# Kernel tuning notes

Measured on AMD Instinct MI355X. Metric: run time of the kernel, lower is better.

The kernel has to match this reference:

```python
import jax, jax.numpy as jnp
import numpy as np

N = 16384          # nodes
E = 262144         # edges (before self-loops)
FIN_N, FIN_E = 768, 64
F, FE = 256, 128   # node/edge channels
H, C = 8, 32       # heads, per-head dim (H*C == F)
L = 2              # num GATv2 modules
NEG_SLOPE = 0.2


def layer_norm(x, g, b, eps=1e-5):
    mu = jnp.mean(x, axis=-1, keepdims=True)
    var = jnp.mean((x - mu) ** 2, axis=-1, keepdims=True)
    return (x - mu) * jax.lax.rsqrt(var + eps) * g + b


def segment_softmax(logits, seg, n):
    # logits: [Et, H], seg: [Et] destination node ids
    m = jax.ops.segment_max(logits, seg, num_segments=n)
    m = jnp.where(jnp.isfinite(m), m, 0.0)
    e = jnp.exp(logits - m[seg])
    s = jax.ops.segment_sum(e, seg, num_segments=n)
    return e / (s[seg] + 1e-16)


def setup_inputs() -> dict:
    key = jax.random.key(0)
    ks = jax.random.split(key, 20)
    inp = {
        "node_feats": jax.random.normal(ks[0], (N, FIN_N), jnp.float32),
        "edge_index": jax.random.randint(ks[1], (2, E), 0, N, dtype=jnp.int32),
        "edge_attr": jax.random.normal(ks[2], (E, FIN_E), jnp.float32),
        # input projections (bias=False)
        "init_node_w": jax.random.normal(ks[3], (F, FIN_N), jnp.float32) * 0.02,
        "init_edge_w": jax.random.normal(ks[4], (FE, FIN_E), jnp.float32) * 0.02,
        # per-layer GATv2 params, stacked on leading layer dim L
        "lin_l_w": jax.random.normal(ks[5], (L, H * C, F), jnp.float32) * 0.05,
        "lin_l_b": jnp.zeros((L, H * C), jnp.float32),
        "lin_r_w": jax.random.normal(ks[6], (L, H * C, F), jnp.float32) * 0.05,
        "lin_r_b": jnp.zeros((L, H * C), jnp.float32),
        "lin_edge_w": jax.random.normal(ks[7], (L, H * C, FE), jnp.float32) * 0.05,
        "att": jax.random.normal(ks[8], (L, H, C), jnp.float32) * 0.05,
        "gat_bias": jnp.zeros((L, H * C), jnp.float32),
        # block params
        "ln1_g": jnp.ones((L, F), jnp.float32), "ln1_b": jnp.zeros((L, F), jnp.float32),
        "mlp_w1": jax.random.normal(ks[9], (L, 2 * F, F), jnp.float32) * 0.05,
        "mlp_w2": jax.random.normal(ks[10], (L, F, 2 * F), jnp.float32) * 0.05,
        "ln2_g": jnp.ones((L, F), jnp.float32), "ln2_b": jnp.zeros((L, F), jnp.float32),
    }
    return inp


def _gatv2_module(x, src, dst, e_emb, p, l, n):
    # e_emb: [Et, H, C] already projected edge embeddings (incl. self-loops)
    x_l = (x @ p["lin_l_w"][l].T + p["lin_l_b"][l]).reshape(n, H, C)
    x_r = (x @ p["lin_r_w"][l].T + p["lin_r_b"][l]).reshape(n, H, C)
    m = x_l[src] + x_r[dst] + e_emb                    # [Et, H, C]
    g = jnp.where(m >= 0, m, NEG_SLOPE * m)            # leaky_relu(0.2)
    logits = jnp.einsum('ehc,hc->eh', g, p["att"][l])
    alpha = segment_softmax(logits, dst, n)            # [Et, H]
    out = jax.ops.segment_sum(alpha[:, :, None] * x_l[src], dst, num_segments=n)
    out = out.reshape(n, H * C) + p["gat_bias"][l]
    # residual -> LN -> MLP -> residual -> LN  (dropout=0, eval mode)
    h = layer_norm(x + out, p["ln1_g"][l], p["ln1_b"][l])
    y = jax.nn.gelu(h @ p["mlp_w1"][l].T, approximate=False) @ p["mlp_w2"][l].T
    return layer_norm(h + y, p["ln2_g"][l], p["ln2_b"][l])


def reference(node_feats, edge_index, edge_attr, init_node_w, init_edge_w,
              lin_l_w, lin_l_b, lin_r_w, lin_r_b, lin_edge_w, att, gat_bias,
              ln1_g, ln1_b, mlp_w1, mlp_w2, ln2_g, ln2_b):
    p = dict(lin_l_w=lin_l_w, lin_l_b=lin_l_b, lin_r_w=lin_r_w, lin_r_b=lin_r_b,
             lin_edge_w=lin_edge_w, att=att, gat_bias=gat_bias, ln1_g=ln1_g,
             ln1_b=ln1_b, mlp_w1=mlp_w1, mlp_w2=mlp_w2, ln2_g=ln2_g, ln2_b=ln2_b)
    x = node_feats @ init_node_w.T                     # [N, F]
    ea = edge_attr @ init_edge_w.T                     # [E, FE]
    src, dst = edge_index[0], edge_index[1]
    # add self loops with fill_value='mean' (mean of incoming edge_attr per node)
    cnt = jax.ops.segment_sum(jnp.ones((E,), ea.dtype), dst, num_segments=N)
    loop_attr = jax.ops.segment_sum(ea, dst, num_segments=N) / jnp.maximum(cnt, 1.0)[:, None]
    ea_all = jnp.concatenate([ea, loop_attr], axis=0)  # [E+N, FE]
    ar = jnp.arange(N, dtype=src.dtype)
    src_all = jnp.concatenate([src, ar])
    dst_all = jnp.concatenate([dst, ar])
    for l in range(L):
        e_emb = (ea_all @ lin_edge_w[l].T).reshape(-1, H, C)
        x = _gatv2_module(x, src_all, dst_all, e_emb, p, l, N)
    return x
```

## Files before the change

### kernel.cpp

```cpp
#include <hip/hip_runtime.h>

typedef unsigned short u16;
typedef __attribute__((ext_vector_type(8))) short s8v;
typedef __attribute__((ext_vector_type(4))) float f4v;

#define NN 16384
#define EE 262144
#define ET (EE + NN)
#define NTILES (ET / 64)

__device__ __forceinline__ float bfu(u16 h){ return __uint_as_float((unsigned)h << 16); }
__device__ __forceinline__ u16 f2bf(float f){
  unsigned u = __float_as_uint(f);
  unsigned r = u + 0x7FFFu + ((u >> 16) & 1u);
  return (u16)(r >> 16);
}
__device__ __forceinline__ float ldf(const void* p, size_t i, int isbf){
  return isbf ? bfu(((const u16*)p)[i]) : ((const float*)p)[i];
}
__device__ __forceinline__ float gelu_f(float x){ return 0.5f*x*(1.0f+erff(x*0.7071067811865475f)); }

__device__ __forceinline__ uint4 load8bf(const void* p, size_t eoff, int isbf){
  if (isbf) return *(const uint4*)((const u16*)p + eoff);
  const float* f = (const float*)p + eoff;
  uint4 r;
  r.x = (unsigned)f2bf(f[0]) | ((unsigned)f2bf(f[1])<<16);
  r.y = (unsigned)f2bf(f[2]) | ((unsigned)f2bf(f[3])<<16);
  r.z = (unsigned)f2bf(f[4]) | ((unsigned)f2bf(f[5])<<16);
  r.w = (unsigned)f2bf(f[6]) | ((unsigned)f2bf(f[7])<<16);
  return r;
}

__device__ __forceinline__ void gload16(const void* g, void* l){
  __builtin_amdgcn_global_load_lds((const __attribute__((address_space(1))) void*)g,
                                   (__attribute__((address_space(3))) void*)l, 16, 0, 0);
}

__global__ void k_detect(const void* nf, int* flag)
{
  int t = threadIdx.x;
  const float* f = (const float*)nf;
  int cnt = 0;
  for (int i = t; i < 4096; i += 256) {
    float a = fabsf(f[i]);
    if (a > 1e-5f && a < 100.0f) cnt++;
  }
  __shared__ int s[256];
  s[t] = cnt; __syncthreads();
  for (int st = 128; st > 0; st >>= 1) { if (t < st) s[t] += s[t+st]; __syncthreads(); }
  if (t == 0) *flag = (s[0] < 2048) ? 1 : 0;
}

__global__ void k_cvt(const void* __restrict__ in, u16* __restrict__ out, const int* __restrict__ dflag)
{
  int isbf = *dflag;
  size_t i = ((size_t)blockIdx.x*256 + threadIdx.x)*8;
  *(uint4*)&out[i] = load8bf(in, i, isbf);
}

__global__ void k_wcvt(const void* __restrict__ lw, const void* __restrict__ rw,
                       const void* __restrict__ w1, const void* __restrict__ w2,
                       const void* __restrict__ iw, u16* __restrict__ wall,
                       const int* __restrict__ dflag)
{
  int isbf = *dflag;
  size_t i = ((size_t)blockIdx.x*256 + threadIdx.x)*8;
  const void* src; size_t off;
  if (i < 196608) { src = iw; off = i; }
  else {
    size_t j = i - 196608;
    size_t l = j / 393216; j -= l*393216;
    if (j < 65536)       { src = lw; off = l*65536 + j; }
    else if (j < 131072) { src = rw; off = l*65536 + (j - 65536); }
    else if (j < 262144) { src = w1; off = l*131072 + (j - 131072); }
    else                 { src = w2; off = l*131072 + (j - 262144); }
  }
  *(uint4*)&wall[i] = load8bf(src, off, isbf);
}

template<int KK, int NJ, int ACT, int CFMT>
__global__ __launch_bounds__(256)
void mg4(const u16* __restrict__ A, const u16* __restrict__ B,
         const void* __restrict__ bias1, const void* __restrict__ bias2,
         size_t bioff, int nsplit, int has_bias,
         void* __restrict__ C, void* __restrict__ C2, int N,
         const int* __restrict__ dflag)
{
  __shared__ u16 As[32][512];
  int isbf = *dflag;
  int t = threadIdx.x;
  int w = t>>6, lane = t&63, l4 = lane&15, quad = lane>>4;

  int nwg = gridDim.x*gridDim.y;
  int wg  = blockIdx.y*gridDim.x + blockIdx.x;
  int lg  = (wg & 7)*(nwg >> 3) + (wg >> 3);
  int bx  = lg % gridDim.x, by = lg / gridDim.x;
  int bm = by*64, bn = bx*(64*NJ);

  const u16* gA = A + (size_t)(bm + w*16 + l4)*KK + quad*8;
  const u16* gB[NJ];
  #pragma unroll
  for (int j=0;j<NJ;++j)
    gB[j] = B + (size_t)(bn + (NJ*w + j)*16 + l4)*KK + quad*8;

  f4v acc[4][NJ];
  f4v zero = {0.f,0.f,0.f,0.f};
  #pragma unroll
  for (int i=0;i<4;++i)
    #pragma unroll
    for (int j=0;j<NJ;++j) acc[i][j] = zero;

  #pragma unroll
  for (int kc=0; kc<KK/256; ++kc) {
    if (kc) __syncthreads();
    s8v breg[8][NJ];
    #pragma unroll
    for (int c=0;c<8;++c)
      #pragma unroll
      for (int j=0;j<NJ;++j)
        breg[c][j] = *(const s8v*)(gB[j] + kc*256 + c*32);
    #pragma unroll
    for (int c=0;c<8;++c)
      gload16(gA + kc*256 + c*32, &As[c*4 + w][0]);
    __syncthreads();
    #pragma unroll
    for (int c=0;c<8;++c) {
      s8v a[4];
      #pragma unroll
      for (int i=0;i<4;++i) a[i] = *(const s8v*)&As[c*4 + i][lane*8];
      #pragma unroll
      for (int i=0;i<4;++i)
        #pragma unroll
        for (int j=0;j<NJ;++j)
          acc[i][j] = __builtin_amdgcn_mfma_f32_16x16x32_bf16(a[i], breg[c][j], acc[i][j], 0,0,0);
    }
  }

  #pragma unroll
  for (int i=0;i<4;++i)
    #pragma unroll
    for (int j=0;j<NJ;++j) {
      int cj = bn + (NJ*w + j)*16 + l4;
      float bvs = 0.f;
      if (has_bias) bvs = (cj < nsplit) ? ldf(bias1, bioff + cj, isbf)
                                        : ldf(bias2, bioff + cj - nsplit, isbf);
      #pragma unroll
      for (int r=0;r<4;++r) {
        int row = bm + i*16 + quad*4 + r;
        float v = acc[i][j][r] + bvs;
        if (ACT==1) v = gelu_f(v);
        if (CFMT==1) ((u16*)C)[(size_t)row*N + cj] = f2bf(v);
        else {
          ((float*)C)[(size_t)row*N + cj] = v;
          if (CFMT==2) ((u16*)C2)[(size_t)row*N + cj] = f2bf(v);
        }
      }
    }
}

__global__ void k_count(const int* __restrict__ dst, int* __restrict__ deg)
{
  int e = blockIdx.x*256 + threadIdx.x;
  if (e >= ET) return;
  int d = (e < EE) ? dst[e] : (e - EE);
  atomicAdd(&deg[d], 1);
}

__global__ void k_scan(const int* __restrict__ deg, int* __restrict__ rowstart)
{
  __shared__ int csum[256];
  int t = threadIdx.x;
  int s = 0;
  for (int i=0;i<64;i++) s += deg[t*64+i];
  csum[t] = s;
  __syncthreads();
  if (t == 0) {
    int r = 0;
    for (int i=0;i<256;i++){ int v = csum[i]; csum[i] = r; r += v; }
    rowstart[NN] = r;
  }
  __syncthreads();
  int b = csum[t];
  for (int i=0;i<64;i++){ rowstart[t*64+i] = b; b += deg[t*64+i]; }
}

__global__ void k_scatter(const int* __restrict__ src, const int* __restrict__ dst,
                          const int* __restrict__ rowstart,
                          int* __restrict__ fill, int* __restrict__ csr,
                          int* __restrict__ srcc, int* __restrict__ dstc)
{
  int e = blockIdx.x*256 + threadIdx.x;
  if (e >= ET) return;
  int d  = (e < EE) ? dst[e] : (e - EE);
  int sv = (e < EE) ? src[e] : (e - EE);
  int pos = rowstart[d] + atomicAdd(&fill[d], 1);
  csr[pos]  = e;
  srcc[pos] = sv;
  dstc[pos] = d;
}

__global__ __launch_bounds__(256)
void k_lm_acsr(const int* __restrict__ csr, const int* __restrict__ rowstart,
               const u16* __restrict__ eab, u16* __restrict__ attr_csr)
{
  int j = threadIdx.x & 63, wid = threadIdx.x >> 6;
  int n = blockIdx.x*4 + wid;
  int s = rowstart[n], e1 = rowstart[n+1];
  float sum = 0.f; int cnt = 0; int selfpos = s;
  for (int p = s; p < e1; ++p) {
    int eid = csr[p];
    if (eid < EE) {
      u16 v = eab[(size_t)eid*64 + j];
      attr_csr[(size_t)p*64 + j] = v;
      sum += bfu(v); cnt++;
    } else selfpos = p;
  }
  attr_csr[(size_t)selfpos*64 + j] = f2bf(sum / (float)max(cnt, 1));
}

__global__ void k_wc(const void* __restrict__ We, const void* __restrict__ iew,
                     u16* __restrict__ Wcb, const int* __restrict__ dflag)
{
  int isbf = *dflag;
  int idx = blockIdx.x*256 + threadIdx.x;
  int j = idx & 63, c = (idx >> 6) & 255, l = idx >> 14;
  float s = 0.f;
  for (int k=0;k<128;k++) s += ldf(We, ((size_t)l*256 + c)*128 + k, isbf) * ldf(iew, (size_t)k*64 + j, isbf);
  Wcb[idx] = f2bf(s);
}

__global__ __launch_bounds__(256)
void k_elogits(const int* __restrict__ srcc, const int* __restrict__ dstc,
               const u16* __restrict__ Wcb, const u16* __restrict__ xlr,
               const u16* __restrict__ attr_csr,
               const void* __restrict__ att, size_t att_off,
               float* __restrict__ logits, const int* __restrict__ dflag)
{
  int isbf = *dflag;
  __shared__ u16 WcF[32*64*8];
  __shared__ u16 attr_s[64*72];
  __shared__ float satt[256];
  __shared__ int ssrc[64], sdst[64];

  int t = threadIdx.x;
  int w = t>>6, lane = t&63, l4 = lane&15, quad = lane>>4;

  satt[t] = ldf(att, att_off + t, isbf);
  #pragma unroll
  for (int f = 0; f < 8; ++f) {
    int fr = w + f*4;
    int i = fr >> 1, ks = fr & 1;
    *(uint4*)&WcF[(fr*64 + lane)*8] = *(const uint4*)&Wcb[(size_t)(16*i + l4)*64 + ks*32 + quad*8];
  }

  f4v zero = {0.f,0.f,0.f,0.f};
  for (int tile = blockIdx.x; tile < NTILES; tile += gridDim.x) {
    int e0 = tile*64;
    __syncthreads();
    if (t < 64) {
      ssrc[t] = srcc[e0 + t];
      sdst[t] = dstc[e0 + t];
    }
    {
      int er = t >> 2, part = t & 3;
      const u16* src = attr_csr + (size_t)(e0 + er)*64 + part*16;
      *(uint4*)&attr_s[er*72 + part*16]     = *(const uint4*)src;
      *(uint4*)&attr_s[er*72 + part*16 + 8] = *(const uint4*)(src + 8);
    }
    __syncthreads();

    s8v b0 = *(const s8v*)&attr_s[(w*16 + l4)*72 + quad*8];
    s8v b1 = *(const s8v*)&attr_s[(w*16 + l4)*72 + 32 + quad*8];
    f4v acc[16];
    #pragma unroll
    for (int i=0;i<16;++i){
      s8v a0 = *(const s8v*)&WcF[((2*i  )*64 + lane)*8];
      s8v a1 = *(const s8v*)&WcF[((2*i+1)*64 + lane)*8];
      acc[i] = __builtin_amdgcn_mfma_f32_16x16x32_bf16(a0, b0, zero, 0,0,0);
      acc[i] = __builtin_amdgcn_mfma_f32_16x16x32_bf16(a1, b1, acc[i], 0,0,0);
    }

    int me = w*16 + l4;
    int sn = ssrc[me], dn = sdst[me];
    float ph[8] = {0.f,0.f,0.f,0.f,0.f,0.f,0.f,0.f};
    #pragma unroll
    for (int i=0;i<16;++i){
      uint2 xlv = *(const uint2*)&xlr[(size_t)sn*512 +       i*16 + quad*4];
      uint2 xrv = *(const uint2*)&xlr[(size_t)dn*512 + 256 + i*16 + quad*4];
      float4 av = *(const float4*)&satt[i*16 + quad*4];
      float m0 = acc[i][0] + bfu((u16)(xlv.x & 0xffff)) + bfu((u16)(xrv.x & 0xffff));
      float m1 = acc[i][1] + bfu((u16)(xlv.x >> 16))    + bfu((u16)(xrv.x >> 16));
      float m2 = acc[i][2] + bfu((u16)(xlv.y & 0xffff)) + bfu((u16)(xrv.y & 0xffff));
      float m3 = acc[i][3] + bfu((u16)(xlv.y >> 16))    + bfu((u16)(xrv.y >> 16));
      float g0 = fmaxf(m0, 0.2f*m0), g1 = fmaxf(m1, 0.2f*m1);
      float g2 = fmaxf(m2, 0.2f*m2), g3 = fmaxf(m3, 0.2f*m3);
      ph[i>>1] += av.x*g0 + av.y*g1 + av.z*g2 + av.w*g3;
    }
    #pragma unroll
    for (int h=0;h<8;++h){
      ph[h] += __shfl_xor(ph[h], 16);
      ph[h] += __shfl_xor(ph[h], 32);
    }
    if (quad == 0){
      float4 lo = {ph[0], ph[1], ph[2], ph[3]};
      float4 hi = {ph[4], ph[5], ph[6], ph[7]};
      *(float4*)&logits[(size_t)(e0 + me)*8]     = lo;
      *(float4*)&logits[(size_t)(e0 + me)*8 + 4] = hi;
    }
  }
}

__global__ __launch_bounds__(256)
void k_aggln(const int* __restrict__ srcc, const int* __restrict__ rowstart,
             const float* __restrict__ logits, const u16* __restrict__ xlr, const float* __restrict__ xbuf,
             const void* __restrict__ gat_bias, const void* __restrict__ ln1g, const void* __restrict__ ln1b,
             size_t poff, float* __restrict__ hbuf, u16* __restrict__ hbufb, const int* __restrict__ dflag)
{
  int isbf = *dflag;
  int lane = threadIdx.x & 63, wid = threadIdx.x >> 6;
  int n = blockIdx.x*4 + wid;
  int s = rowstart[n], deg = rowstart[n+1] - s;
  int myh = lane >> 3;
  float mrun = -3.0e38f, lrun = 0.f;
  float a0=0.f, a1=0.f, a2=0.f, a3=0.f;

  for (int c0 = 0; c0 < deg; c0 += 64) {
    int idx = s + c0 + lane; if (idx >= ET) idx = ET-1;
    int sv = srcc[idx];
    int lim = min(64, deg - c0);
    size_t lbase = (size_t)(s + c0)*8 + myh;
    for (int j = 0; j < lim; ++j) {
      int sn  = __shfl(sv, j);
      float lg = logits[lbase + (size_t)j*8];
      uint2 xv = *(const uint2*)&xlr[(size_t)sn*512 + 4*lane];
      float mn = fmaxf(mrun, lg);
      float sc = __expf(mrun - mn);
      float wv = __expf(lg - mn);
      mrun = mn;
      lrun = lrun*sc + wv;
      a0 = a0*sc + wv*bfu((u16)(xv.x & 0xffff));
      a1 = a1*sc + wv*bfu((u16)(xv.x >> 16));
      a2 = a2*sc + wv*bfu((u16)(xv.y & 0xffff));
      a3 = a3*sc + wv*bfu((u16)(xv.y >> 16));
    }
  }
  float inv = 1.f/(lrun + 1e-16f);
  int c = 4*lane;
  float4 res = *(const float4*)&xbuf[(size_t)n*256 + c];
  float o0 = a0*inv + ldf(gat_bias, poff+c+0, isbf) + res.x;
  float o1 = a1*inv + ldf(gat_bias, poff+c+1, isbf) + res.y;
  float o2 = a2*inv + ldf(gat_bias, poff+c+2, isbf) + res.z;
  float o3 = a3*inv + ldf(gat_bias, poff+c+3, isbf) + res.w;

  float v = o0+o1+o2+o3;
  #pragma unroll
  for (int off=1; off<64; off<<=1) v += __shfl_xor(v, off);
  float mu = v * (1.f/256.f);
  float d0=o0-mu, d1=o1-mu, d2=o2-mu, d3=o3-mu;
  float v2 = d0*d0+d1*d1+d2*d2+d3*d3;
  #pragma unroll
  for (int off=1; off<64; off<<=1) v2 += __shfl_xor(v2, off);
  float wn = rsqrtf(v2*(1.f/256.f) + 1e-5f);
  float4 outv;
  outv.x = d0*wn*ldf(ln1g, poff+c+0, isbf) + ldf(ln1b, poff+c+0, isbf);
  outv.y = d1*wn*ldf(ln1g, poff+c+1, isbf) + ldf(ln1b, poff+c+1, isbf);
  outv.z = d2*wn*ldf(ln1g, poff+c+2, isbf) + ldf(ln1b, poff+c+2, isbf);
  outv.w = d3*wn*ldf(ln1g, poff+c+3, isbf) + ldf(ln1b, poff+c+3, isbf);
  *(float4*)&hbuf[(size_t)n*256 + c] = outv;
  uint2 hb;
  hb.x = (unsigned)f2bf(outv.x) | ((unsigned)f2bf(outv.y)<<16);
  hb.y = (unsigned)f2bf(outv.z) | ((unsigned)f2bf(outv.w)<<16);
  *(uint2*)&hbufb[(size_t)n*256 + c] = hb;
}

__global__ __launch_bounds__(256)
void k_ln_add(const float* __restrict__ a, const u16* __restrict__ b2,
              const void* __restrict__ gg, const void* __restrict__ bb, size_t poff,
              float* __restrict__ out, u16* __restrict__ outb, const int* __restrict__ dflag)
{
  int isbf = *dflag;
  int n = blockIdx.x, t = threadIdx.x;
  __shared__ float r[256];
  float x = a[(size_t)n*256 + t] + bfu(b2[(size_t)n*256 + t]);
  r[t] = x; __syncthreads();
  for (int st = 128; st > 0; st >>= 1) { if (t < st) r[t] += r[t+st]; __syncthreads(); }
  float mu = r[0] * (1.f/256.f);
  __syncthreads();
  float d = x - mu;
  r[t] = d*d; __syncthreads();
  for (int st = 128; st > 0; st >>= 1) { if (t < st) r[t] += r[t+st]; __syncthreads(); }
  float var = r[0] * (1.f/256.f);
  float o = d * rsqrtf(var + 1e-5f) * ldf(gg, poff + t, isbf) + ldf(bb, poff + t, isbf);
  out[(size_t)n*256 + t] = o;
  outb[(size_t)n*256 + t] = f2bf(o);
}

__global__ void k_out(const float* __restrict__ x, void* __restrict__ out, const int* __restrict__ dflag)
{
  int isbf = *dflag;
  int i = blockIdx.x*256 + threadIdx.x;
  if (isbf) ((u16*)out)[i] = f2bf(x[i]);
  else      ((float*)out)[i] = x[i];
}

extern "C" void kernel_launch(void* const* d_in, const int* in_sizes, int n_in,
                              void* d_out, int out_size, void* d_ws, size_t ws_size,
                              hipStream_t stream)
{
  const void* node_feats = d_in[0];
  const int*  edge_index = (const int*)d_in[1];
  const void* edge_attr  = d_in[2];
  const void* init_node_w= d_in[3];
  const void* init_edge_w= d_in[4];
  const void* lin_l_w    = d_in[5];
  const void* lin_l_b    = d_in[6];
  const void* lin_r_w    = d_in[7];
  const void* lin_r_b    = d_in[8];
  const void* lin_edge_w = d_in[9];
  const void* att        = d_in[10];
  const void* gat_bias   = d_in[11];
  const void* ln1_g      = d_in[12];
  const void* ln1_b      = d_in[13];
  const void* mlp_w1     = d_in[14];
  const void* mlp_w2     = d_in[15];
  const void* ln2_g      = d_in[16];
  const void* ln2_b      = d_in[17];

  const int* srcp = edge_index;
  const int* dstp = edge_index + EE;

  char* p = (char*)d_ws;
  auto alloc = [&](size_t bytes) { void* r = (void*)p; p += (bytes + 255) & ~(size_t)255; return r; };
  int*   dflag   = (int*)alloc(256);
  int*   deg     = (int*)alloc((size_t)NN*4);
  int*   rowstart= (int*)alloc((size_t)(NN+1)*4);
  int*   fill    = (int*)alloc((size_t)NN*4);
  int*   csr     = (int*)alloc((size_t)ET*4);
  int*   srcc    = (int*)alloc((size_t)ET*4);
  int*   dstc    = (int*)alloc((size_t)ET*4);
  u16*   Wcb     = (u16*)alloc((size_t)2*256*64*2);
  u16*   wall    = (u16*)alloc((size_t)983040*2);
  u16*   attr_csr= (u16*)alloc((size_t)ET*64*2);
  float* logits  = (float*)alloc((size_t)ET*8*4);
  float* hbuf    = (float*)alloc((size_t)NN*256*4);
  float* xbuf    = (float*)alloc((size_t)NN*256*4);
  u16*   xbufb   = (u16*)alloc((size_t)NN*256*2);
  u16*   hbufb   = (u16*)alloc((size_t)NN*256*2);
  u16*   xlr     = (u16*)alloc((size_t)NN*512*2);
  u16*   eab     = (u16*)logits;
  u16*   nfb     = (u16*)logits;
  u16*   ymid    = xlr;
  u16*   y2      = (u16*)d_out;

  u16* Wn = wall;

  hipMemsetAsync(deg,  0, (size_t)NN*4, stream);
  hipMemsetAsync(fill, 0, (size_t)NN*4, stream);

  k_detect <<<1, 256, 0, stream>>>(node_feats, dflag);

  k_count  <<<(ET+255)/256, 256, 0, stream>>>(dstp, deg);
  k_scan   <<<1, 256, 0, stream>>>(deg, rowstart);
  k_scatter<<<(ET+255)/256, 256, 0, stream>>>(srcp, dstp, rowstart, fill, csr, srcc, dstc);
  k_cvt    <<<(EE*64)/(8*256), 256, 0, stream>>>(edge_attr, eab, dflag);
  k_lm_acsr<<<NN/4, 256, 0, stream>>>(csr, rowstart, eab, attr_csr);

  k_wc     <<<128, 256, 0, stream>>>(lin_edge_w, init_edge_w, Wcb, dflag);
  k_wcvt   <<<480, 256, 0, stream>>>(lin_l_w, lin_r_w, mlp_w1, mlp_w2, init_node_w, wall, dflag);

  k_cvt<<<(NN*768)/(8*256), 256, 0, stream>>>(node_feats, nfb, dflag);
  mg4<768,1,0,2><<<dim3(4, NN/64), 256, 0, stream>>>(nfb, Wn, nullptr, nullptr, 0, 1<<29, 0,
                                                     xbuf, xbufb, 256, dflag);

  for (int l = 0; l < 2; ++l) {
    size_t bo = (size_t)l*256;
    u16* Wlr = wall + 196608 + (size_t)l*393216;
    u16* W1  = Wlr + 131072;
    u16* W2  = Wlr + 262144;
    mg4<256,2,0,1><<<dim3(4, NN/64), 256, 0, stream>>>(xbufb, Wlr, lin_l_b, lin_r_b, bo, 256, 1,
                                                       xlr, nullptr, 512, dflag);
    k_elogits<<<768, 256, 0, stream>>>(srcc, dstc, Wcb + (size_t)l*256*64, xlr,
                                       attr_csr, att, (size_t)l*256, logits, dflag);
    k_aggln<<<NN/4, 256, 0, stream>>>(srcc, rowstart, logits, xlr, xbuf,
                                      gat_bias, ln1_g, ln1_b, bo, hbuf, hbufb, dflag);
    mg4<256,2,1,1><<<dim3(4, NN/64), 256, 0, stream>>>(hbufb, W1, nullptr, nullptr, 0, 1<<29, 0,
                                                       ymid, nullptr, 512, dflag);
    mg4<512,1,0,1><<<dim3(4, NN/64), 256, 0, stream>>>(ymid, W2, nullptr, nullptr, 0, 1<<29, 0,
                                                       y2, nullptr, 256, dflag);
    k_ln_add<<<NN, 256, 0, stream>>>(hbuf, y2, ln2_g, ln2_b, bo, xbuf, xbufb, dflag);
  }

  k_out<<<(NN*256)/256, 256, 0, stream>>>(xbuf, d_out, dflag);
}
```

Measured before the change: 671.9 us.

## Fuse edge_attr conversion into CSR gather and drop LDS staging in elogits

Removes the separate k_cvt pass over edge_attr, so k_lm_acsr reads the raw input and converts to bf16 as it gathers into CSR order. This saves one full write and re-read of the edge attributes. In k_elogits each lane now loads its own src/dst indices and attr operands straight from global memory rather than staging a tile in shared memory, which removes two barriers per tile. The grid grows from 768 to 1024 blocks. The trade-off is that the gather becomes uncoalesced on fp32 input, and the direct global loads in elogits are less coalesced.

Measured after the change: 714.3 us. 1.06x slower.

```diff
diff --git a/kernel.cpp b/kernel.cpp
--- a/kernel.cpp
+++ b/kernel.cpp
@@ -201,8 +201,10 @@
 
 __global__ __launch_bounds__(256)
 void k_lm_acsr(const int* __restrict__ csr, const int* __restrict__ rowstart,
-               const u16* __restrict__ eab, u16* __restrict__ attr_csr)
-{
+               const void* __restrict__ edge_attr, u16* __restrict__ attr_csr,
+               const int* __restrict__ dflag)
+{
+  int isbf = *dflag;
   int j = threadIdx.x & 63, wid = threadIdx.x >> 6;
   int n = blockIdx.x*4 + wid;
   int s = rowstart[n], e1 = rowstart[n+1];
@@ -210,9 +212,9 @@
   for (int p = s; p < e1; ++p) {
     int eid = csr[p];
     if (eid < EE) {
-      u16 v = eab[(size_t)eid*64 + j];
-      attr_csr[(size_t)p*64 + j] = v;
-      sum += bfu(v); cnt++;
+      float v = ldf(edge_attr, (size_t)eid*64 + j, isbf);
+      attr_csr[(size_t)p*64 + j] = f2bf(v);
+      sum += v; cnt++;
     } else selfpos = p;
   }
   attr_csr[(size_t)selfpos*64 + j] = f2bf(sum / (float)max(cnt, 1));
@@ -238,9 +240,7 @@
 {
   int isbf = *dflag;
   __shared__ u16 WcF[32*64*8];
-  __shared__ u16 attr_s[64*72];
   __shared__ float satt[256];
-  __shared__ int ssrc[64], sdst[64];
 
   int t = threadIdx.x;
   int w = t>>6, lane = t&63, l4 = lane&15, quad = lane>>4;
@@ -252,25 +252,16 @@
     int i = fr >> 1, ks = fr & 1;
     *(uint4*)&WcF[(fr*64 + lane)*8] = *(const uint4*)&Wcb[(size_t)(16*i + l4)*64 + ks*32 + quad*8];
   }
+  __syncthreads();
 
   f4v zero = {0.f,0.f,0.f,0.f};
+  int me = w*16 + l4;
   for (int tile = blockIdx.x; tile < NTILES; tile += gridDim.x) {
-    int e0 = tile*64;
-    __syncthreads();
-    if (t < 64) {
-      ssrc[t] = srcc[e0 + t];
-      sdst[t] = dstc[e0 + t];
-    }
-    {
-      int er = t >> 2, part = t & 3;
-      const u16* src = attr_csr + (size_t)(e0 + er)*64 + part*16;
-      *(uint4*)&attr_s[er*72 + part*16]     = *(const uint4*)src;
-      *(uint4*)&attr_s[er*72 + part*16 + 8] = *(const uint4*)(src + 8);
-    }
-    __syncthreads();
-
-    s8v b0 = *(const s8v*)&attr_s[(w*16 + l4)*72 + quad*8];
-    s8v b1 = *(const s8v*)&attr_s[(w*16 + l4)*72 + 32 + quad*8];
+    int epos = tile*64 + me;
+    int sn = srcc[epos], dn = dstc[epos];
+    s8v b0 = *(const s8v*)&attr_csr[(size_t)epos*64 + quad*8];
+    s8v b1 = *(const s8v*)&attr_csr[(size_t)epos*64 + 32 + quad*8];
+
     f4v acc[16];
     #pragma unroll
     for (int i=0;i<16;++i){
@@ -280,8 +271,6 @@
       acc[i] = __builtin_amdgcn_mfma_f32_16x16x32_bf16(a1, b1, acc[i], 0,0,0);
     }
 
-    int me = w*16 + l4;
-    int sn = ssrc[me], dn = sdst[me];
     float ph[8] = {0.f,0.f,0.f,0.f,0.f,0.f,0.f,0.f};
     #pragma unroll
     for (int i=0;i<16;++i){
@@ -304,8 +293,8 @@
     if (quad == 0){
       float4 lo = {ph[0], ph[1], ph[2], ph[3]};
       float4 hi = {ph[4], ph[5], ph[6], ph[7]};
-      *(float4*)&logits[(size_t)(e0 + me)*8]     = lo;
-      *(float4*)&logits[(size_t)(e0 + me)*8 + 4] = hi;
+      *(float4*)&logits[(size_t)epos*8]     = lo;
+      *(float4*)&logits[(size_t)epos*8 + 4] = hi;
     }
   }
 }
@@ -447,7 +436,6 @@
   u16*   xbufb   = (u16*)alloc((size_t)NN*256*2);
   u16*   hbufb   = (u16*)alloc((size_t)NN*256*2);
   u16*   xlr     = (u16*)alloc((size_t)NN*512*2);
-  u16*   eab     = (u16*)logits;
   u16*   nfb     = (u16*)logits;
   u16*   ymid    = xlr;
   u16*   y2      = (u16*)d_out;
@@ -462,8 +450,7 @@
   k_count  <<<(ET+255)/256, 256, 0, stream>>>(dstp, deg);
   k_scan   <<<1, 256, 0, stream>>>(deg, rowstart);
   k_scatter<<<(ET+255)/256, 256, 0, stream>>>(srcp, dstp, rowstart, fill, csr, srcc, dstc);
-  k_cvt    <<<(EE*64)/(8*256), 256, 0, stream>>>(edge_attr, eab, dflag);
-  k_lm_acsr<<<NN/4, 256, 0, stream>>>(csr, rowstart, eab, attr_csr);
+  k_lm_acsr<<<NN/4, 256, 0, stream>>>(csr, rowstart, edge_attr, attr_csr, dflag);
 
   k_wc     <<<128, 256, 0, stream>>>(lin_edge_w, init_edge_w, Wcb, dflag);
   k_wcvt   <<<480, 256, 0, stream>>>(lin_l_w, lin_r_w, mlp_w1, mlp_w2, init_node_w, wall, dflag);
@@ -479,8 +466,8 @@
     u16* W2  = Wlr + 262144;
     mg4<256,2,0,1><<<dim3(4, NN/64), 256, 0, stream>>>(xbufb, Wlr, lin_l_b, lin_r_b, bo, 256, 1,
                                                        xlr, nullptr, 512, dflag);
-    k_elogits<<<768, 256, 0, stream>>>(srcc, dstc, Wcb + (size_t)l*256*64, xlr,
-                                       attr_csr, att, (size_t)l*256, logits, dflag);
+    k_elogits<<<1024, 256, 0, stream>>>(srcc, dstc, Wcb + (size_t)l*256*64, xlr,
+                                        attr_csr, att, (size_t)l*256, logits, dflag);
     k_aggln<<<NN/4, 256, 0, stream>>>(srcc, rowstart, logits, xlr, xbuf,
                                       gat_bias, ln1_g, ln1_b, bo, hbuf, hbufb, dflag);
     mg4<256,2,1,1><<<dim3(4, NN/64), 256, 0, stream>>>(hbufb, W1, nullptr, nullptr, 0, 1<<29, 0,
```
